# Kernel optimization log

Measured on AMD Instinct MI355X. Metric: run time of the kernel, lower is better.

## Reference

```python
import jax, jax.numpy as jnp
import numpy as np

EMBED_DIM = 1024
NUM_HEADS = 16
HEAD_DIM = EMBED_DIM // NUM_HEADS


def setup_inputs() -> dict:
    key = jax.random.key(0)
    ks = jax.random.split(key, 9)
    B, S, E = 2, 2048, EMBED_DIM
    scale = 1.0 / np.sqrt(E)
    inputs = jax.random.normal(ks[0], (B, S, E), dtype=jnp.float32)
    # torch nn.Linear params: weight [out,in], bias [out]
    Wq = jax.random.uniform(ks[1], (E, E), jnp.float32, -scale, scale)
    bq = jax.random.uniform(ks[2], (E,), jnp.float32, -scale, scale)
    Wk = jax.random.uniform(ks[3], (E, E), jnp.float32, -scale, scale)
    bk = jax.random.uniform(ks[4], (E,), jnp.float32, -scale, scale)
    Wv = jax.random.uniform(ks[5], (E, E), jnp.float32, -scale, scale)
    bv = jax.random.uniform(ks[6], (E,), jnp.float32, -scale, scale)
    Wo = jax.random.uniform(ks[7], (E, E), jnp.float32, -scale, scale)
    bo = jax.random.uniform(ks[8], (E,), jnp.float32, -scale, scale)
    return {"inputs": inputs, "Wq": Wq, "bq": bq, "Wk": Wk, "bk": bk,
            "Wv": Wv, "bv": bv, "Wo": Wo, "bo": bo}


def _split_heads(x, B, S):
    # [B,S,E] -> [B,H,S,Dh]
    return x.reshape(B, S, NUM_HEADS, HEAD_DIM).transpose(0, 2, 1, 3)


def reference(inputs, Wq, bq, Wk, bk, Wv, bv, Wo, bo):
    B, S, E = inputs.shape
    q = _split_heads(inputs @ Wq.T + bq, B, S)
    k = _split_heads(inputs @ Wk.T + bk, B, S)
    v = _split_heads(inputs @ Wv.T + bv, B, S)
    inv_sqrt_dk = 1.0 / jnp.sqrt(jnp.float32(HEAD_DIM))
    scores = jnp.einsum('bhqd,bhkd->bhqk', q, k) * inv_sqrt_dk
    weights = jax.nn.softmax(scores, axis=-1)
    attn = jnp.einsum('bhqk,bhkd->bhqd', weights, v)
    concat = attn.transpose(0, 2, 1, 3).reshape(B, S, E)
    return concat @ Wo.T + bo
```

## Files before the change

### kernel.cpp

```cpp
#include <hip/hip_runtime.h>
#include <hip/hip_bf16.h>
#include <stdint.h>


typedef short bf16x8 __attribute__((ext_vector_type(8)));
typedef float f32x4 __attribute__((ext_vector_type(4)));

__device__ __forceinline__ unsigned short f2b(float x) {
    unsigned b = __float_as_uint(x);
    b += 0x7FFFu + ((b >> 16) & 1u);
    return (unsigned short)(b >> 16);
}
__device__ __forceinline__ float b2f(unsigned short u) {
    return __uint_as_float(((unsigned)u) << 16);
}
__device__ __forceinline__ f32x4 mfma16(bf16x8 a, bf16x8 b, f32x4 c) {
    return __builtin_amdgcn_mfma_f32_16x16x32_bf16(a, b, c, 0, 0, 0);
}
__device__ __forceinline__ void gl16(const void* g, void* l) {
    __builtin_amdgcn_global_load_lds(
        (const __attribute__((address_space(1))) void*)g,
        (__attribute__((address_space(3))) void*)l, 16, 0, 0);
}

__global__ void round_kernel(const float* __restrict__ src,
                             unsigned short* __restrict__ dst, int n4) {
    int i = blockIdx.x * blockDim.x + threadIdx.x;
    if (i >= n4) return;
    float4 v = reinterpret_cast<const float4*>(src)[i];
    ushort4 h;
    h.x = f2b(v.x); h.y = f2b(v.y); h.z = f2b(v.z); h.w = f2b(v.w);
    reinterpret_cast<ushort4*>(dst)[i] = h;
}

__global__ void split_kernel(const float* __restrict__ src,
                             unsigned short* __restrict__ hi,
                             unsigned short* __restrict__ lo, int n4) {
    int i = blockIdx.x * blockDim.x + threadIdx.x;
    if (i >= n4) return;
    float4 v = reinterpret_cast<const float4*>(src)[i];
    ushort4 h, l;
    h.x = f2b(v.x); l.x = f2b(v.x - b2f(h.x));
    h.y = f2b(v.y); l.y = f2b(v.y - b2f(h.y));
    h.z = f2b(v.z); l.z = f2b(v.z - b2f(h.z));
    h.w = f2b(v.w); l.w = f2b(v.w - b2f(h.w));
    reinterpret_cast<ushort4*>(hi)[i] = h;
    reinterpret_cast<ushort4*>(lo)[i] = l;
}

__global__ __launch_bounds__(256, 2)
void gemm_qkv(const unsigned short* __restrict__ Xh, const unsigned short* __restrict__ Wh,
              const float* __restrict__ bias,
              unsigned short* __restrict__ Qs,
              unsigned short* __restrict__ Kh,
              unsigned short* __restrict__ Vh) {
    __shared__ __align__(16) unsigned short sA[128][32];
    __shared__ __align__(16) unsigned short sB[128][32];

    const int tid = threadIdx.x;
    const int lane = tid & 63;
    const int wid = tid >> 6;
    const int wr = wid >> 1, wc = wid & 1;
    const int m0 = blockIdx.y * 128, n0 = blockIdx.x * 128;
    const int fr = lane & 15;
    const int fo = (lane >> 4) << 3;
    const int rgrp = lane >> 4;
    constexpr float SC = 0.18033688011112042f;

    f32x4 zero4 = {0.f, 0.f, 0.f, 0.f};
    f32x4 acc[4][4];
#pragma unroll
    for (int i = 0; i < 4; i++)
#pragma unroll
        for (int j = 0; j < 4; j++) acc[i][j] = zero4;

    for (int k0 = 0; k0 < 1024; k0 += 32) {
        __syncthreads();
#pragma unroll
        for (int q = 0; q < 2; q++) {
            const int u = q * 256 + tid;
            const int row = u >> 2, c = u & 3;
            gl16(Xh + (size_t)(m0 + row) * 1024 + k0 + c * 8, (char*)&sA[0][0] + u * 16);
            gl16(Wh + (size_t)(n0 + row) * 1024 + k0 + c * 8, (char*)&sB[0][0] + u * 16);
        }
        __syncthreads();

        bf16x8 aF[4], bF[4];
#pragma unroll
        for (int i = 0; i < 4; i++) {
            aF[i] = *(const bf16x8*)&sA[wr * 64 + i * 16 + fr][fo];
            bF[i] = *(const bf16x8*)&sB[wc * 64 + i * 16 + fr][fo];
        }
#pragma unroll
        for (int i = 0; i < 4; i++)
#pragma unroll
            for (int j = 0; j < 4; j++)
                acc[i][j] = mfma16(aF[i], bF[j], acc[i][j]);
    }

#pragma unroll
    for (int i = 0; i < 4; i++) {
#pragma unroll
        for (int j = 0; j < 4; j++) {
            const int col = n0 + wc * 64 + j * 16 + fr;
            const float bv = bias[col];
            const int which = col >> 10;
            const int nn = col & 1023;
            const int h = nn >> 6, d = nn & 63;
#pragma unroll
            for (int r = 0; r < 4; r++) {
                const int row = m0 + wr * 64 + i * 16 + rgrp * 4 + r;
                const float v = acc[i][j][r] + bv;
                const int b = row >> 11, s = row & 2047;
                const size_t o = (((size_t)(b * 16 + h)) * 2048 + s) * 64 + d;
                if (which == 0)      Qs[o] = f2b(v * SC);
                else if (which == 1) Kh[o] = f2b(v);
                else                 Vh[o] = f2b(v);
            }
        }
    }
}

__global__ __launch_bounds__(256)
void vtrans(const unsigned short* __restrict__ V, unsigned short* __restrict__ Vt) {
    __shared__ unsigned short L[64][72];
    const int t = threadIdx.x;
    const int bh = blockIdx.y, s0 = blockIdx.x * 64;
    const size_t ib = (size_t)bh * 2048 * 64;
    const int srow = t >> 2, sc = (t & 3) * 16;
    *(uint4*)&L[srow][sc]     = *(const uint4*)(V + ib + (size_t)(s0 + srow) * 64 + sc);
    *(uint4*)&L[srow][sc + 8] = *(const uint4*)(V + ib + (size_t)(s0 + srow) * 64 + sc + 8);
    __syncthreads();
    const int d = t >> 2, k0 = (t & 3) * 16;
    unsigned short tmp[16];
#pragma unroll
    for (int i = 0; i < 16; i++) tmp[i] = L[k0 + i][d];
    *(uint4*)(Vt + ib + (size_t)d * 2048 + s0 + k0)     = *(uint4*)&tmp[0];
    *(uint4*)(Vt + ib + (size_t)d * 2048 + s0 + k0 + 8) = *(uint4*)&tmp[8];
}

__global__ __launch_bounds__(512)
void attn_kernel(const unsigned short* __restrict__ Qs,
                 const unsigned short* __restrict__ Kh,
                 const unsigned short* __restrict__ Vt,
                 unsigned short* __restrict__ OutHi, unsigned short* __restrict__ OutLo) {
    __shared__ __align__(16) unsigned short sK[2][64][64];
    __shared__ __align__(16) unsigned short sV[2][64][64];
    __shared__ __align__(16) unsigned short sP[8][16][72];

    const int tid = threadIdx.x, lane = tid & 63, wid = tid >> 6;
    const int bh = blockIdx.y;
    const int q0 = blockIdx.x * 128;
    const int fr = lane & 15, fo = (lane >> 4) << 3, rgrp = lane >> 4;
    const size_t baseQK = (size_t)bh * 2048 * 64;
    const size_t baseVt = (size_t)bh * 64 * 2048;

    bf16x8 ones;
#pragma unroll
    for (int i = 0; i < 8; i++) ones[i] = (short)0x3F80;

    const int srow = tid >> 3, sc = tid & 7;
    const int lofs = srow * 128 + ((sc ^ (srow & 7)) << 4);

    bf16x8 qh[2];
    {
        const size_t qoff = baseQK + (size_t)(q0 + wid * 16 + fr) * 64;
        qh[0] = *(const bf16x8*)(Qs + qoff + fo);
        qh[1] = *(const bf16x8*)(Qs + qoff + 32 + fo);
    }

    f32x4 zero4 = {0.f, 0.f, 0.f, 0.f};
    f32x4 accO[4], accL = zero4;
#pragma unroll
    for (int i = 0; i < 4; i++) accO[i] = zero4;
    float mrow[4] = {-INFINITY, -INFINITY, -INFINITY, -INFINITY};

    auto ldsw = [&](const unsigned short* S, int row, int c) -> bf16x8 {
        return *(const bf16x8*)((const char*)S + row * 128 + ((c ^ (row & 7)) << 4));
    };

    uint4 kreg, vreg;
    kreg = *(const uint4*)(Kh + baseQK + (size_t)srow * 64 + sc * 8);
    vreg = *(const uint4*)(Vt + baseVt + (size_t)srow * 2048 + sc * 8);
    *(uint4*)((char*)&sK[0][0][0] + lofs) = kreg;
    *(uint4*)((char*)&sV[0][0][0] + lofs) = vreg;
    __syncthreads();

    int cur = 0;
    for (int kt = 0; kt < 2048; kt += 64) {
        const bool more = (kt + 64) < 2048;
        if (more) {
            kreg = *(const uint4*)(Kh + baseQK + (size_t)(kt + 64 + srow) * 64 + sc * 8);
            vreg = *(const uint4*)(Vt + baseVt + (size_t)srow * 2048 + kt + 64 + sc * 8);
        }

        const unsigned short* sKc = &sK[cur][0][0];
        const unsigned short* sVc = &sV[cur][0][0];

        f32x4 s4[4];
#pragma unroll
        for (int nf = 0; nf < 4; nf++) {
            const int kr_ = nf * 16 + fr;
            f32x4 sa = mfma16(qh[0], ldsw(sKc, kr_, rgrp), zero4);
            sa = mfma16(qh[1], ldsw(sKc, kr_, 4 + rgrp), sa);
            s4[nf] = sa;
        }

        float scl[4];
#pragma unroll
        for (int r = 0; r < 4; r++) {
            float v = fmaxf(fmaxf(s4[0][r], s4[1][r]), fmaxf(s4[2][r], s4[3][r]));
            v = fmaxf(v, __shfl_xor(v, 1));
            v = fmaxf(v, __shfl_xor(v, 2));
            v = fmaxf(v, __shfl_xor(v, 4));
            v = fmaxf(v, __shfl_xor(v, 8));
            const float mnew = fmaxf(mrow[r], v);
            scl[r] = exp2f(mrow[r] - mnew);
            mrow[r] = mnew;
        }
#pragma unroll
        for (int df = 0; df < 4; df++) {
            f32x4 a = accO[df];
            a[0] *= scl[0]; a[1] *= scl[1]; a[2] *= scl[2]; a[3] *= scl[3];
            accO[df] = a;
        }
        accL[0] *= scl[0]; accL[1] *= scl[1]; accL[2] *= scl[2]; accL[3] *= scl[3];

#pragma unroll
        for (int nf = 0; nf < 4; nf++) {
#pragma unroll
            for (int r = 0; r < 4; r++) {
                const float pv = exp2f(s4[nf][r] - mrow[r]);
                const unsigned u = __float_as_uint(pv) + 0x8000u;
                sP[wid][rgrp * 4 + r][nf * 16 + fr] = (unsigned short)(u >> 16);
            }
        }
        __syncthreads();

        bf16x8 pH[2];
        pH[0] = *(const bf16x8*)&sP[wid][fr][fo];
        pH[1] = *(const bf16x8*)&sP[wid][fr][32 + fo];
#pragma unroll
        for (int df = 0; df < 4; df++) {
            const int vrw = df * 16 + fr;
            f32x4 a = accO[df];
            a = mfma16(pH[0], ldsw(sVc, vrw, rgrp), a);
            a = mfma16(pH[1], ldsw(sVc, vrw, 4 + rgrp), a);
            accO[df] = a;
        }
        accL = mfma16(pH[0], ones, accL);
        accL = mfma16(pH[1], ones, accL);

        if (more) {
            *(uint4*)((char*)&sK[cur ^ 1][0][0] + lofs) = kreg;
            *(uint4*)((char*)&sV[cur ^ 1][0][0] + lofs) = vreg;
        }
        __syncthreads();
        cur ^= 1;
    }

    const int b = bh >> 4, h = bh & 15;
#pragma unroll
    for (int df = 0; df < 4; df++) {
#pragma unroll
        for (int r = 0; r < 4; r++) {
            const int s = q0 + wid * 16 + rgrp * 4 + r;
            const int d = df * 16 + fr;
            const float v = accO[df][r] / accL[r];
            const size_t o = ((size_t)(b * 2048 + s)) * 1024 + h * 64 + d;
            const unsigned short hv = f2b(v);
            OutHi[o] = hv;
            OutLo[o] = f2b(v - b2f(hv));
        }
    }
}

__global__ __launch_bounds__(256, 2)
void gemm_out(const unsigned short* __restrict__ Ahi, const unsigned short* __restrict__ Alo,
              const unsigned short* __restrict__ Bhi, const unsigned short* __restrict__ Blo,
              const float* __restrict__ bias, float* __restrict__ outF) {
    __shared__ __align__(16) unsigned short sAh[128][32];
    __shared__ __align__(16) unsigned short sAl[128][32];
    __shared__ __align__(16) unsigned short sBh[128][32];
    __shared__ __align__(16) unsigned short sBl[128][32];

    const int tid = threadIdx.x;
    const int lane = tid & 63;
    const int wid = tid >> 6;
    const int wr = wid >> 1, wc = wid & 1;
    const int m0 = blockIdx.y * 128, n0 = blockIdx.x * 128;
    const int fr = lane & 15;
    const int fo = (lane >> 4) << 3;
    const int rgrp = lane >> 4;

    f32x4 zero4 = {0.f, 0.f, 0.f, 0.f};
    f32x4 acc[4][4];
#pragma unroll
    for (int i = 0; i < 4; i++)
#pragma unroll
        for (int j = 0; j < 4; j++) acc[i][j] = zero4;

    for (int k0 = 0; k0 < 1024; k0 += 32) {
        __syncthreads();
#pragma unroll
        for (int q = 0; q < 2; q++) {
            const int u = (wid * 2 + q) * 64 + lane;
            const int row = u >> 2, cs = u & 3;
            const size_t ga = (size_t)(m0 + row) * 1024 + k0 + cs * 8;
            const size_t gb = (size_t)(n0 + row) * 1024 + k0 + cs * 8;
            gl16(Ahi + ga, (char*)&sAh[0][0] + u * 16);
            gl16(Alo + ga, (char*)&sAl[0][0] + u * 16);
            gl16(Bhi + gb, (char*)&sBh[0][0] + u * 16);
            gl16(Blo + gb, (char*)&sBl[0][0] + u * 16);
        }
        __syncthreads();

        bf16x8 aH[4], aL[4], bH[4], bL[4];
#pragma unroll
        for (int i = 0; i < 4; i++) {
            aH[i] = *(const bf16x8*)&sAh[wr * 64 + i * 16 + fr][fo];
            aL[i] = *(const bf16x8*)&sAl[wr * 64 + i * 16 + fr][fo];
            bH[i] = *(const bf16x8*)&sBh[wc * 64 + i * 16 + fr][fo];
            bL[i] = *(const bf16x8*)&sBl[wc * 64 + i * 16 + fr][fo];
        }
#pragma unroll
        for (int i = 0; i < 4; i++)
#pragma unroll
            for (int j = 0; j < 4; j++) {
                acc[i][j] = mfma16(aH[i], bH[j], acc[i][j]);
                acc[i][j] = mfma16(aH[i], bL[j], acc[i][j]);
                acc[i][j] = mfma16(aL[i], bH[j], acc[i][j]);
            }
    }

#pragma unroll
    for (int i = 0; i < 4; i++) {
#pragma unroll
        for (int j = 0; j < 4; j++) {
            const int col = n0 + wc * 64 + j * 16 + fr;
            const float bv = bias[col];
#pragma unroll
            for (int r = 0; r < 4; r++) {
                const int row = m0 + wr * 64 + i * 16 + rgrp * 4 + r;
                outF[(size_t)row * 1024 + col] = acc[i][j][r] + bv;
            }
        }
    }
}

extern "C" void kernel_launch(void* const* d_in, const int* in_sizes, int n_in,
                              void* d_out, int out_size, void* d_ws, size_t ws_size,
                              hipStream_t stream) {
    const float* X  = (const float*)d_in[0];
    const float* Wq = (const float*)d_in[1];
    const float* bq = (const float*)d_in[2];
    const float* Wk = (const float*)d_in[3];
    const float* bk = (const float*)d_in[4];
    const float* Wv = (const float*)d_in[5];
    const float* bv = (const float*)d_in[6];
    const float* Wo = (const float*)d_in[7];
    const float* bo = (const float*)d_in[8];
    float* out = (float*)d_out;

    char* ws = (char*)d_ws;
    size_t off = 0;
    auto alloc = [&](size_t bytes) -> char* {
        char* p = ws + off;
        off += (bytes + 255) & ~(size_t)255;
        return p;
    };
    const size_t ME = (size_t)4096 * 1024;
    unsigned short* Xh     = (unsigned short*)alloc(ME * 2);
    unsigned short* Wqkvh  = (unsigned short*)alloc((size_t)3072 * 1024 * 2);
    unsigned short* Woh    = (unsigned short*)alloc((size_t)1024 * 1024 * 2);
    unsigned short* Wol    = (unsigned short*)alloc((size_t)1024 * 1024 * 2);
    float*          bqkv   = (float*)alloc(3072 * 4);
    unsigned short* Qsc    = (unsigned short*)alloc(ME * 2);
    unsigned short* Khb    = (unsigned short*)alloc(ME * 2);
    unsigned short* Vhb    = (unsigned short*)alloc(ME * 2);
    unsigned short* Vtb    = (unsigned short*)alloc(ME * 2);
    unsigned short* ATh    = (unsigned short*)alloc(ME * 2);
    unsigned short* ATl    = (unsigned short*)alloc(ME * 2);

    round_kernel<<<4096, 256, 0, stream>>>(X, Xh, (int)(ME / 4));
    round_kernel<<<1024, 256, 0, stream>>>(Wq, Wqkvh, 262144);
    round_kernel<<<1024, 256, 0, stream>>>(Wk, Wqkvh + 1024 * 1024, 262144);
    round_kernel<<<1024, 256, 0, stream>>>(Wv, Wqkvh + 2 * 1024 * 1024, 262144);
    split_kernel<<<1024, 256, 0, stream>>>(Wo, Woh, Wol, 262144);
    hipMemcpyAsync(bqkv,        bq, 4096, hipMemcpyDeviceToDevice, stream);
    hipMemcpyAsync(bqkv + 1024, bk, 4096, hipMemcpyDeviceToDevice, stream);
    hipMemcpyAsync(bqkv + 2048, bv, 4096, hipMemcpyDeviceToDevice, stream);

    gemm_qkv<<<dim3(24, 32), 256, 0, stream>>>(Xh, Wqkvh, bqkv, Qsc, Khb, Vhb);

    vtrans<<<dim3(32, 32), 256, 0, stream>>>(Vhb, Vtb);

    attn_kernel<<<dim3(16, 32), 512, 0, stream>>>(Qsc, Khb, Vtb, ATh, ATl);

    gemm_out<<<dim3(8, 32), 256, 0, stream>>>(ATh, ATl, Woh, Wol, bo, out);
}
```

Before: 284.0 us.

## Keep softmax probabilities in registers via transposed MFMA and fuse rounding kernels

The attention kernel swaps the MFMA operand order so scores come out transposed, with each lane holding a single query row. The probabilities can then be packed straight into bf16 MFMA operands in registers, which removes the sP shared-memory round trip and one __syncthreads per tile. The row sum becomes a plain register sum instead of MFMAs against a ones vector, and the V tile gets a new LDS layout to match the new operand order. The four fp32-to-bf16 rounding launches are also merged into one kernel to cut launch overhead.

```diff
diff --git a/kernel.cpp b/kernel.cpp
--- a/kernel.cpp
+++ b/kernel.cpp
@@ -23,14 +23,28 @@
         (__attribute__((address_space(3))) void*)l, 16, 0, 0);
 }
 
-__global__ void round_kernel(const float* __restrict__ src,
-                             unsigned short* __restrict__ dst, int n4) {
-    int i = blockIdx.x * blockDim.x + threadIdx.x;
-    if (i >= n4) return;
-    float4 v = reinterpret_cast<const float4*>(src)[i];
+__global__ __launch_bounds__(256)
+void round4_kernel(const float* __restrict__ X, const float* __restrict__ Wq,
+                   const float* __restrict__ Wk, const float* __restrict__ Wv,
+                   unsigned short* __restrict__ Xh, unsigned short* __restrict__ Wh) {
+    int i = blockIdx.x * 256 + threadIdx.x;
+    const float4* src;
+    ushort4* dst;
+    if (i < 1048576) {
+        src = (const float4*)X + i;
+        dst = (ushort4*)Xh + i;
+    } else {
+        const int j = i - 1048576;
+        const int w = j >> 18;
+        const int k = j & 262143;
+        const float* S = (w == 0) ? Wq : (w == 1) ? Wk : Wv;
+        src = (const float4*)S + k;
+        dst = (ushort4*)Wh + j;
+    }
+    float4 v = *src;
     ushort4 h;
     h.x = f2b(v.x); h.y = f2b(v.y); h.z = f2b(v.z); h.w = f2b(v.w);
-    reinterpret_cast<ushort4*>(dst)[i] = h;
+    *dst = h;
 }
 
 __global__ void split_kernel(const float* __restrict__ src,
@@ -146,7 +160,6 @@
                  unsigned short* __restrict__ OutHi, unsigned short* __restrict__ OutLo) {
     __shared__ __align__(16) unsigned short sK[2][64][64];
     __shared__ __align__(16) unsigned short sV[2][64][64];
-    __shared__ __align__(16) unsigned short sP[8][16][72];
 
     const int tid = threadIdx.x, lane = tid & 63, wid = tid >> 6;
     const int bh = blockIdx.y;
@@ -155,12 +168,12 @@
     const size_t baseQK = (size_t)bh * 2048 * 64;
     const size_t baseVt = (size_t)bh * 64 * 2048;
 
-    bf16x8 ones;
-#pragma unroll
-    for (int i = 0; i < 8; i++) ones[i] = (short)0x3F80;
-
     const int srow = tid >> 3, sc = tid & 7;
-    const int lofs = srow * 128 + ((sc ^ (srow & 7)) << 4);
+    const int klofs = srow * 128 + ((sc ^ (srow & 7)) << 4);
+    const int cc0 = 4 * (sc >> 2) + 2 * (sc & 1);
+    const int vbyte = 8 * ((sc >> 1) & 1);
+    const int vlofs0 = srow * 128 + ((cc0 ^ (srow & 7)) << 4) + vbyte;
+    const int vlofs1 = srow * 128 + (((cc0 + 1) ^ (srow & 7)) << 4) + vbyte;
 
     bf16x8 qh[2];
     {
@@ -170,10 +183,10 @@
     }
 
     f32x4 zero4 = {0.f, 0.f, 0.f, 0.f};
-    f32x4 accO[4], accL = zero4;
+    f32x4 accO[4];
 #pragma unroll
     for (int i = 0; i < 4; i++) accO[i] = zero4;
-    float mrow[4] = {-INFINITY, -INFINITY, -INFINITY, -INFINITY};
+    float accL = 0.f, mrow = -INFINITY;
 
     auto ldsw = [&](const unsigned short* S, int row, int c) -> bf16x8 {
         return *(const bf16x8*)((const char*)S + row * 128 + ((c ^ (row & 7)) << 4));
@@ -182,8 +195,9 @@
     uint4 kreg, vreg;
     kreg = *(const uint4*)(Kh + baseQK + (size_t)srow * 64 + sc * 8);
     vreg = *(const uint4*)(Vt + baseVt + (size_t)srow * 2048 + sc * 8);
-    *(uint4*)((char*)&sK[0][0][0] + lofs) = kreg;
-    *(uint4*)((char*)&sV[0][0][0] + lofs) = vreg;
+    *(uint4*)((char*)&sK[0][0][0] + klofs) = kreg;
+    *(uint2*)((char*)&sV[0][0][0] + vlofs0) = make_uint2(vreg.x, vreg.y);
+    *(uint2*)((char*)&sV[0][0][0] + vlofs1) = make_uint2(vreg.z, vreg.w);
     __syncthreads();
 
     int cur = 0;
@@ -201,72 +215,82 @@
 #pragma unroll
         for (int nf = 0; nf < 4; nf++) {
             const int kr_ = nf * 16 + fr;
-            f32x4 sa = mfma16(qh[0], ldsw(sKc, kr_, rgrp), zero4);
-            sa = mfma16(qh[1], ldsw(sKc, kr_, 4 + rgrp), sa);
+            f32x4 sa = mfma16(ldsw(sKc, kr_, rgrp), qh[0], zero4);
+            sa = mfma16(ldsw(sKc, kr_, 4 + rgrp), qh[1], sa);
             s4[nf] = sa;
         }
 
-        float scl[4];
-#pragma unroll
-        for (int r = 0; r < 4; r++) {
-            float v = fmaxf(fmaxf(s4[0][r], s4[1][r]), fmaxf(s4[2][r], s4[3][r]));
-            v = fmaxf(v, __shfl_xor(v, 1));
-            v = fmaxf(v, __shfl_xor(v, 2));
-            v = fmaxf(v, __shfl_xor(v, 4));
-            v = fmaxf(v, __shfl_xor(v, 8));
-            const float mnew = fmaxf(mrow[r], v);
-            scl[r] = exp2f(mrow[r] - mnew);
-            mrow[r] = mnew;
-        }
+        float vmax = fmaxf(
+            fmaxf(fmaxf(fmaxf(s4[0][0], s4[0][1]), fmaxf(s4[0][2], s4[0][3])),
+                  fmaxf(fmaxf(s4[1][0], s4[1][1]), fmaxf(s4[1][2], s4[1][3]))),
+            fmaxf(fmaxf(fmaxf(s4[2][0], s4[2][1]), fmaxf(s4[2][2], s4[2][3])),
+                  fmaxf(fmaxf(s4[3][0], s4[3][1]), fmaxf(s4[3][2], s4[3][3]))));
+        vmax = fmaxf(vmax, __shfl_xor(vmax, 16));
+        vmax = fmaxf(vmax, __shfl_xor(vmax, 32));
+        const float mnew = fmaxf(mrow, vmax);
+        const float scl = exp2f(mrow - mnew);
+        mrow = mnew;
+
+        float psum = 0.f;
+        unsigned w[8];
+#pragma unroll
+        for (int nf = 0; nf < 4; nf++) {
+            const float p0 = exp2f(s4[nf][0] - mnew);
+            const float p1 = exp2f(s4[nf][1] - mnew);
+            const float p2 = exp2f(s4[nf][2] - mnew);
+            const float p3 = exp2f(s4[nf][3] - mnew);
+            psum += (p0 + p1) + (p2 + p3);
+            const unsigned t0 = __float_as_uint(p0) + 0x8000u;
+            const unsigned t1 = __float_as_uint(p1) + 0x8000u;
+            const unsigned t2 = __float_as_uint(p2) + 0x8000u;
+            const unsigned t3 = __float_as_uint(p3) + 0x8000u;
+            w[nf * 2]     = __builtin_amdgcn_perm(t1, t0, 0x07060302u);
+            w[nf * 2 + 1] = __builtin_amdgcn_perm(t3, t2, 0x07060302u);
+        }
+        psum += __shfl_xor(psum, 16);
+        psum += __shfl_xor(psum, 32);
+        accL = accL * scl + psum;
 #pragma unroll
         for (int df = 0; df < 4; df++) {
             f32x4 a = accO[df];
-            a[0] *= scl[0]; a[1] *= scl[1]; a[2] *= scl[2]; a[3] *= scl[3];
+            a[0] *= scl; a[1] *= scl; a[2] *= scl; a[3] *= scl;
             accO[df] = a;
         }
-        accL[0] *= scl[0]; accL[1] *= scl[1]; accL[2] *= scl[2]; accL[3] *= scl[3];
-
-#pragma unroll
-        for (int nf = 0; nf < 4; nf++) {
-#pragma unroll
-            for (int r = 0; r < 4; r++) {
-                const float pv = exp2f(s4[nf][r] - mrow[r]);
-                const unsigned u = __float_as_uint(pv) + 0x8000u;
-                sP[wid][rgrp * 4 + r][nf * 16 + fr] = (unsigned short)(u >> 16);
-            }
-        }
-        __syncthreads();
-
-        bf16x8 pH[2];
-        pH[0] = *(const bf16x8*)&sP[wid][fr][fo];
-        pH[1] = *(const bf16x8*)&sP[wid][fr][32 + fo];
+
+        uint4 pw0 = {w[0], w[1], w[2], w[3]};
+        uint4 pw1 = {w[4], w[5], w[6], w[7]};
+        bf16x8 pf0 = *reinterpret_cast<bf16x8*>(&pw0);
+        bf16x8 pf1 = *reinterpret_cast<bf16x8*>(&pw1);
+
 #pragma unroll
         for (int df = 0; df < 4; df++) {
             const int vrw = df * 16 + fr;
             f32x4 a = accO[df];
-            a = mfma16(pH[0], ldsw(sVc, vrw, rgrp), a);
-            a = mfma16(pH[1], ldsw(sVc, vrw, 4 + rgrp), a);
+            a = mfma16(ldsw(sVc, vrw, rgrp), pf0, a);
+            a = mfma16(ldsw(sVc, vrw, 4 + rgrp), pf1, a);
             accO[df] = a;
         }
-        accL = mfma16(pH[0], ones, accL);
-        accL = mfma16(pH[1], ones, accL);
 
         if (more) {
-            *(uint4*)((char*)&sK[cur ^ 1][0][0] + lofs) = kreg;
-            *(uint4*)((char*)&sV[cur ^ 1][0][0] + lofs) = vreg;
+            char* kb = (char*)&sK[cur ^ 1][0][0];
+            char* vb = (char*)&sV[cur ^ 1][0][0];
+            *(uint4*)(kb + klofs) = kreg;
+            *(uint2*)(vb + vlofs0) = make_uint2(vreg.x, vreg.y);
+            *(uint2*)(vb + vlofs1) = make_uint2(vreg.z, vreg.w);
         }
         __syncthreads();
         cur ^= 1;
     }
 
     const int b = bh >> 4, h = bh & 15;
+    const int s = q0 + wid * 16 + fr;
+    const float rL = 1.0f / accL;
 #pragma unroll
     for (int df = 0; df < 4; df++) {
 #pragma unroll
         for (int r = 0; r < 4; r++) {
-            const int s = q0 + wid * 16 + rgrp * 4 + r;
-            const int d = df * 16 + fr;
-            const float v = accO[df][r] / accL[r];
+            const int d = df * 16 + rgrp * 4 + r;
+            const float v = accO[df][r] * rL;
             const size_t o = ((size_t)(b * 2048 + s)) * 1024 + h * 64 + d;
             const unsigned short hv = f2b(v);
             OutHi[o] = hv;
@@ -382,10 +406,7 @@
     unsigned short* ATh    = (unsigned short*)alloc(ME * 2);
     unsigned short* ATl    = (unsigned short*)alloc(ME * 2);
 
-    round_kernel<<<4096, 256, 0, stream>>>(X, Xh, (int)(ME / 4));
-    round_kernel<<<1024, 256, 0, stream>>>(Wq, Wqkvh, 262144);
-    round_kernel<<<1024, 256, 0, stream>>>(Wk, Wqkvh + 1024 * 1024, 262144);
-    round_kernel<<<1024, 256, 0, stream>>>(Wv, Wqkvh + 2 * 1024 * 1024, 262144);
+    round4_kernel<<<7168, 256, 0, stream>>>(X, Wq, Wk, Wv, Xh, Wqkvh);
     split_kernel<<<1024, 256, 0, stream>>>(Wo, Woh, Wol, 262144);
     hipMemcpyAsync(bqkv,        bq, 4096, hipMemcpyDeviceToDevice, stream);
     hipMemcpyAsync(bqkv + 1024, bk, 4096, hipMemcpyDeviceToDevice, stream);
```

Result: faster. 259.5 us (-8.6%).
